# Optimization experiments

Measured on AMD Instinct MI355X. Metric: run time of the kernel, lower is better.

## Reference

```python
import jax, jax.numpy as jnp
import numpy as np

TAU = 0.8
LAMBDA_BALANCE = 0.05
EPS = 1e-8


def setup_inputs() -> dict:
    key = jax.random.key(0)
    ks = jax.random.split(key, 8)
    B, Din, Dh, Dout, E = 8192, 1024, 2048, 1024, 8
    x = jax.random.normal(ks[0], (B, Din), jnp.float32)
    # gumbel noise for F.gumbel_softmax: g = -log(-log(U)), U~Uniform(0,1)
    u = jax.random.uniform(ks[1], (B, E), jnp.float32, 1e-6, 1.0 - 1e-6)
    gumbel = -jnp.log(-jnp.log(u))
    gate_w = jax.random.normal(ks[2], (Din, E), jnp.float32) * 0.02
    gate_b = jnp.zeros((E,), jnp.float32)
    w1 = jax.random.normal(ks[3], (E, Din, Dh), jnp.float32) * (1.0 / np.sqrt(Din))
    b1 = jnp.zeros((E, Dh), jnp.float32)
    w2 = jax.random.normal(ks[4], (E, Dh, Dout), jnp.float32) * (1.0 / np.sqrt(Dh))
    b2 = jnp.zeros((E, Dout), jnp.float32)
    return dict(x=x, gumbel=gumbel, gate_w=gate_w, gate_b=gate_b,
                w1=w1, b1=b1, w2=w2, b2=b2)


def reference(x, gumbel, gate_w, gate_b, w1, b1, w2, b2):
    # gating logits [B, E]
    logits = x @ gate_w + gate_b
    # gumbel-softmax (soft), tau=0.8 -> selection probs (selection_policy='soft')
    probs = jax.nn.softmax((logits + gumbel) / TAU, axis=1)
    # load-balancing auxiliary loss
    router_probs = jax.nn.softmax(logits / TAU, axis=1)
    importance = router_probs.mean(axis=0)  # [E]
    load = probs.mean(axis=0)               # [E]
    importance_cv = jnp.std(importance, ddof=1) / (importance.mean() + EPS)
    load_cv = jnp.std(load, ddof=1) / (load.mean() + EPS)
    E = probs.shape[1]
    switch_loss = E * jnp.sum(importance * load)
    aux_loss = (switch_loss + importance_cv + load_cv) * LAMBDA_BALANCE
    # dense all-expert MLP stack: h [E,B,Dh], eo [E,B,Dout]
    h = jax.nn.relu(jnp.einsum('bd,edh->ebh', x, w1) + b1[:, None, :])
    eo = jnp.einsum('ebh,eho->ebo', h, w2) + b2[:, None, :]
    # bmm combine: expert_outputs [B, Dout, E] @ probs [B, E, 1] -> [B, Dout]
    output = jnp.einsum('ebo,be->bo', eo, probs)
    return output, aux_loss
```

## Files before the change

kernel.cpp:

```cpp
#include <hip/hip_runtime.h>

typedef __attribute__((ext_vector_type(4))) float f4;
typedef __attribute__((ext_vector_type(8))) short s8;

__device__ inline float b2f(unsigned int u) {
    unsigned int v = u << 16;
    float f;
    __builtin_memcpy(&f, &v, 4);
    return f;
}
__device__ inline unsigned short f2b(float f) {
    unsigned int u;
    __builtin_memcpy(&u, &f, 4);
    unsigned int r = u + 0x7fffu + ((u >> 16) & 1u);
    return (unsigned short)(r >> 16);
}
__device__ inline void async16(const void* g, void* l) {
    __builtin_amdgcn_global_load_lds(
        (const __attribute__((address_space(1))) unsigned int*)g,
        (__attribute__((address_space(3))) unsigned int*)l, 16, 0, 0);
}

#define B_ROWS 8192
#define DIN 1024
#define DH 2048
#define DOUT 1024
#define NE 8
#define NCAT 16384

__global__ __launch_bounds__(64) void detect_dtype(const unsigned short* __restrict__ p, int* __restrict__ flag)
{
    const int lane = threadIdx.x;
    int sane = 0;
    for (int i = lane; i < 4096; i += 64) {
        const float a = fabsf(b2f(p[i]));
        if (a > 1e-30f && a < 1e3f) sane++;
    }
    for (int off = 32; off; off >>= 1) sane += __shfl_xor(sane, off, 64);
    if (lane == 0) *flag = (sane < 3600) ? 1 : 0;
}

__global__ __launch_bounds__(256) void normalize_kernel(const void* __restrict__ src,
                                                        unsigned short* __restrict__ dst,
                                                        const int* __restrict__ flag, int n)
{
    const int i = blockIdx.x * 256 + threadIdx.x;
    if (i >= n) return;
    if (*flag) dst[i] = f2b(((const float*)src)[i]);
    else       dst[i] = ((const unsigned short*)src)[i];
}

__global__ __launch_bounds__(256) void gating_kernel(
    const unsigned short* __restrict__ x, const unsigned short* __restrict__ gum,
    const unsigned short* __restrict__ gw, const unsigned short* __restrict__ gb,
    float* __restrict__ probs, float* __restrict__ partials)
{
    const int t = threadIdx.x, wave = t >> 6, lane = t & 63;
    float sp = 0.f, sr = 0.f;
    const int base = blockIdx.x * 32 + wave * 8;
    for (int rr = 0; rr < 8; rr++) {
        const int b = base + rr;
        float acc[8];
#pragma unroll
        for (int e = 0; e < 8; e++) acc[e] = 0.f;
        for (int kk = 0; kk < 16; kk++) {
            const int k = kk * 64 + lane;
            const float xv = b2f(x[(size_t)b * DIN + k]);
            const uint4 wv = *(const uint4*)(gw + (size_t)k * 8);
            acc[0] += xv * b2f(wv.x & 0xffffu); acc[1] += xv * b2f(wv.x >> 16);
            acc[2] += xv * b2f(wv.y & 0xffffu); acc[3] += xv * b2f(wv.y >> 16);
            acc[4] += xv * b2f(wv.z & 0xffffu); acc[5] += xv * b2f(wv.z >> 16);
            acc[6] += xv * b2f(wv.w & 0xffffu); acc[7] += xv * b2f(wv.w >> 16);
        }
#pragma unroll
        for (int e = 0; e < 8; e++)
            for (int off = 32; off; off >>= 1) acc[e] += __shfl_xor(acc[e], off, 64);
        float lg[8], p1[8], p2[8];
        float m1 = -1e30f, m2 = -1e30f;
#pragma unroll
        for (int e = 0; e < 8; e++) {
            lg[e] = acc[e] + b2f(gb[e]);
            p1[e] = (lg[e] + b2f(gum[(size_t)b * 8 + e])) * 1.25f;
            p2[e] = lg[e] * 1.25f;
            m1 = fmaxf(m1, p1[e]); m2 = fmaxf(m2, p2[e]);
        }
        float s1 = 0.f, s2 = 0.f;
#pragma unroll
        for (int e = 0; e < 8; e++) {
            p1[e] = expf(p1[e] - m1); s1 += p1[e];
            p2[e] = expf(p2[e] - m2); s2 += p2[e];
        }
        const float i1 = 1.f / s1, i2 = 1.f / s2;
        if (lane < 8) {
            const float pv = p1[lane] * i1;
            probs[(size_t)b * 8 + lane] = pv;
            sp += pv;
            sr += p2[lane] * i2;
        }
    }
    __shared__ float red[4][16];
    if (lane < 8) { red[wave][lane] = sp; red[wave][8 + lane] = sr; }
    __syncthreads();
    if (t < 16)
        partials[blockIdx.x * 16 + t] = red[0][t] + red[1][t] + red[2][t] + red[3][t];
}

__global__ void aux_finalize(const float* __restrict__ partials, void* __restrict__ outp,
                             const int* __restrict__ flag)
{
    __shared__ float fin[16];
    const int t = threadIdx.x;
    if (t < 16) {
        float s = 0.f;
        for (int i = 0; i < 256; i++) s += partials[i * 16 + t];
        fin[t] = s;
    }
    __syncthreads();
    if (t == 0) {
        float ld[8], im[8];
        for (int e = 0; e < 8; e++) { ld[e] = fin[e] / 8192.f; im[e] = fin[8 + e] / 8192.f; }
        float mi = 0.f, ml = 0.f;
        for (int e = 0; e < 8; e++) { mi += im[e]; ml += ld[e]; }
        mi *= 0.125f; ml *= 0.125f;
        float vi = 0.f, vl = 0.f, sw = 0.f;
        for (int e = 0; e < 8; e++) {
            vi += (im[e] - mi) * (im[e] - mi);
            vl += (ld[e] - ml) * (ld[e] - ml);
            sw += im[e] * ld[e];
        }
        const float cvi = sqrtf(vi / 7.f) / (mi + 1e-8f);
        const float cvl = sqrtf(vl / 7.f) / (ml + 1e-8f);
        const float aux = (8.f * sw + cvi + cvl) * 0.05f;
        if (*flag) ((float*)outp)[8388608] = aux;
        else       ((unsigned short*)outp)[8388608] = f2b(aux);
    }
}

__global__ __launch_bounds__(256) void transpose_cvt(
    const void* __restrict__ src, unsigned short* __restrict__ out,
    int R, int C, int ldOut, size_t outEStride, const int* __restrict__ flag)
{
    __shared__ unsigned short tile[64][65];
    const int e = blockIdx.z;
    const size_t eoff = (size_t)e * R * C;
    unsigned short* op = out + (size_t)e * outEStride;
    const int fl = *flag;
    const int tx = threadIdx.x, ty = threadIdx.y;
    const int r0 = blockIdx.y * 64, c0 = blockIdx.x * 64;
    if (fl) {
        const float* in = (const float*)src + eoff;
#pragma unroll
        for (int i = 0; i < 16; i++) {
            const int r = ty + i * 4;
            tile[r][tx] = f2b(in[(size_t)(r0 + r) * C + c0 + tx]);
        }
    } else {
        const unsigned short* in = (const unsigned short*)src + eoff;
#pragma unroll
        for (int i = 0; i < 16; i++) {
            const int r = ty + i * 4;
            tile[r][tx] = in[(size_t)(r0 + r) * C + c0 + tx];
        }
    }
    __syncthreads();
#pragma unroll
    for (int i = 0; i < 16; i++) {
        const int c = ty + i * 4;
        op[(size_t)(c0 + c) * ldOut + r0 + tx] = tile[tx][c];
    }
}

__global__ __launch_bounds__(256) void gemm_h(
    const unsigned short* __restrict__ A,
    const unsigned short* __restrict__ Bt,
    const unsigned short* __restrict__ bias,
    const float* __restrict__ probs,
    unsigned short* __restrict__ outH)
{
    constexpr int K = DIN;
    __shared__ __align__(16) char smem[32768];

    const int t = threadIdx.x;
    const int m0 = blockIdx.x * 128, n0 = blockIdx.y * 128;
    const int wave = t >> 6, lane = t & 63;
    const int wm = wave >> 1, wn = wave & 1;
    const int quad = lane >> 4, l16 = lane & 15;

    f4 acc[4][4];
#pragma unroll
    for (int i = 0; i < 4; i++)
#pragma unroll
        for (int j = 0; j < 4; j++) { acc[i][j][0] = 0.f; acc[i][j][1] = 0.f; acc[i][j][2] = 0.f; acc[i][j][3] = 0.f; }

    const int rA = t >> 2;
    const int cb = (t & 3) * 16;
    const char* pA0 = (const char*)(A + (size_t)(m0 + rA) * K) + cb;
    const char* pA1 = pA0 + (size_t)64 * K * 2;
    const char* pB0 = (const char*)(Bt + (size_t)(n0 + rA) * K) + cb;
    const char* pB1 = pB0 + (size_t)64 * K * 2;

    int aoff[4], boff[4];
#pragma unroll
    for (int i = 0; i < 4; i++) {
        aoff[i] = ((wm * 64 + i * 16 + l16) * 32 + quad * 8) * 2;
        boff[i] = ((wn * 64 + i * 16 + l16) * 32 + quad * 8) * 2;
    }

    auto stage = [&](int buf, int k0) {
        const size_t kb = (size_t)k0 * 2;
        char* s = smem + buf * 16384;
        async16(pA0 + kb, s + t * 16);
        async16(pA1 + kb, s + 4096 + t * 16);
        async16(pB0 + kb, s + 8192 + t * 16);
        async16(pB1 + kb, s + 12288 + t * 16);
    };

    stage(0, 0);
    __syncthreads();
    int cur = 0;
    for (int k0 = 0; k0 < K; k0 += 32) {
        if (k0 + 32 < K) stage(cur ^ 1, k0 + 32);
        const char* s = smem + cur * 16384;
        s8 av[4], bv[4];
#pragma unroll
        for (int i = 0; i < 4; i++) av[i] = *(const s8*)(s + aoff[i]);
#pragma unroll
        for (int j = 0; j < 4; j++) bv[j] = *(const s8*)(s + 8192 + boff[j]);
#pragma unroll
        for (int i = 0; i < 4; i++)
#pragma unroll
            for (int j = 0; j < 4; j++)
                acc[i][j] = __builtin_amdgcn_mfma_f32_16x16x32_bf16(av[i], bv[j], acc[i][j], 0, 0, 0);
        __syncthreads();
        cur ^= 1;
    }

#pragma unroll
    for (int i = 0; i < 4; i++) {
        const int gmB = m0 + wm * 64 + i * 16 + quad * 4;
#pragma unroll
        for (int j = 0; j < 4; j++) {
            const int gn = n0 + wn * 64 + j * 16 + l16;
            const int e = gn >> 11;
            const float bval = b2f(bias[gn]);
#pragma unroll
            for (int r = 0; r < 4; r++) {
                const int gm = gmB + r;
                const float pb = probs[(size_t)gm * 8 + e];
                float v = acc[i][j][r] + bval;
                v = fmaxf(v, 0.f) * pb;
                outH[(size_t)gm * NCAT + gn] = f2b(v);
            }
        }
    }
}

__global__ __launch_bounds__(256) void gemm_out_sk(
    const unsigned short* __restrict__ A,
    const unsigned short* __restrict__ Bt,
    float* __restrict__ partial, int rows)
{
    constexpr int K = NCAT;
    __shared__ __align__(16) char smem[32768];

    const int t = threadIdx.x;
    const int m0 = blockIdx.x * 128, n0 = blockIdx.y * 128;
    const int nks = gridDim.z;
    const int klen = K / nks;
    const int kstart = blockIdx.z * klen;
    const int kend = kstart + klen;
    const int wave = t >> 6, lane = t & 63;
    const int wm = wave >> 1, wn = wave & 1;
    const int quad = lane >> 4, l16 = lane & 15;

    f4 acc[4][4];
#pragma unroll
    for (int i = 0; i < 4; i++)
#pragma unroll
        for (int j = 0; j < 4; j++) { acc[i][j][0] = 0.f; acc[i][j][1] = 0.f; acc[i][j][2] = 0.f; acc[i][j][3] = 0.f; }

    const int rA = t >> 2;
    const int cb = (t & 3) * 16;
    const char* pA0 = (const char*)(A + (size_t)(m0 + rA) * K) + cb;
    const char* pA1 = pA0 + (size_t)64 * K * 2;
    const char* pB0 = (const char*)(Bt + (size_t)(n0 + rA) * K) + cb;
    const char* pB1 = pB0 + (size_t)64 * K * 2;

    int aoff[4], boff[4];
#pragma unroll
    for (int i = 0; i < 4; i++) {
        aoff[i] = ((wm * 64 + i * 16 + l16) * 32 + quad * 8) * 2;
        boff[i] = ((wn * 64 + i * 16 + l16) * 32 + quad * 8) * 2;
    }

    auto stage = [&](int buf, int k0) {
        const size_t kb = (size_t)k0 * 2;
        char* s = smem + buf * 16384;
        async16(pA0 + kb, s + t * 16);
        async16(pA1 + kb, s + 4096 + t * 16);
        async16(pB0 + kb, s + 8192 + t * 16);
        async16(pB1 + kb, s + 12288 + t * 16);
    };

    stage(0, kstart);
    __syncthreads();
    int cur = 0;
    for (int k0 = kstart; k0 < kend; k0 += 32) {
        if (k0 + 32 < kend) stage(cur ^ 1, k0 + 32);
        const char* s = smem + cur * 16384;
        s8 av[4], bv[4];
#pragma unroll
        for (int i = 0; i < 4; i++) av[i] = *(const s8*)(s + aoff[i]);
#pragma unroll
        for (int j = 0; j < 4; j++) bv[j] = *(const s8*)(s + 8192 + boff[j]);
#pragma unroll
        for (int i = 0; i < 4; i++)
#pragma unroll
            for (int j = 0; j < 4; j++)
                acc[i][j] = __builtin_amdgcn_mfma_f32_16x16x32_bf16(av[i], bv[j], acc[i][j], 0, 0, 0);
        __syncthreads();
        cur ^= 1;
    }

    float* pp = partial + (size_t)blockIdx.z * rows * DOUT;
#pragma unroll
    for (int i = 0; i < 4; i++) {
        const int gmB = m0 + wm * 64 + i * 16 + quad * 4;
#pragma unroll
        for (int j = 0; j < 4; j++) {
            const int gn = n0 + wn * 64 + j * 16 + l16;
#pragma unroll
            for (int r = 0; r < 4; r++)
                pp[(size_t)(gmB + r) * DOUT + gn] = acc[i][j][r];
        }
    }
}

__global__ __launch_bounds__(256) void out_finalize(
    const float* __restrict__ partial, const unsigned short* __restrict__ b2,
    const float* __restrict__ probs, void* __restrict__ outp, size_t outOff,
    const int* __restrict__ flag, int rows, int nks)
{
    const int idx = blockIdx.x * 256 + threadIdx.x;
    if (idx >= rows * DOUT) return;
    const int m = idx >> 10, n = idx & (DOUT - 1);
    float v = 0.f;
    for (int ks = 0; ks < nks; ks++)
        v += partial[(size_t)ks * rows * DOUT + idx];
    const f4 p0 = *(const f4*)(probs + (size_t)m * 8);
    const f4 p1 = *(const f4*)(probs + (size_t)m * 8 + 4);
    v += p0[0] * b2f(b2[n])            + p0[1] * b2f(b2[DOUT + n])
       + p0[2] * b2f(b2[2 * DOUT + n]) + p0[3] * b2f(b2[3 * DOUT + n])
       + p1[0] * b2f(b2[4 * DOUT + n]) + p1[1] * b2f(b2[5 * DOUT + n])
       + p1[2] * b2f(b2[6 * DOUT + n]) + p1[3] * b2f(b2[7 * DOUT + n]);
    const size_t oi = outOff + ((size_t)m * DOUT) + n;
    if (*flag) ((float*)outp)[oi] = v;
    else       ((unsigned short*)outp)[oi] = f2b(v);
}

extern "C" void kernel_launch(void* const* d_in, const int* in_sizes, int n_in,
                              void* d_out, int out_size, void* d_ws, size_t ws_size,
                              hipStream_t stream)
{
    const void* x   = d_in[0];
    const void* gum = d_in[1];
    const void* gw  = d_in[2];
    const void* gb  = d_in[3];
    const void* w1  = d_in[4];
    const void* b1  = d_in[5];
    const void* w2  = d_in[6];
    const void* b2  = d_in[7];

    char* ws = (char*)d_ws;
    size_t cur = 0;
    auto alloc = [&](size_t bytes) { size_t p = cur; cur = (cur + bytes + 255) & ~(size_t)255; return p; };

    int* flag              = (int*)(ws + alloc(256));
    float* probs           = (float*)(ws + alloc(8192 * 8 * 4));
    float* partials        = (float*)(ws + alloc(256 * 16 * 4));
    unsigned short* xn     = (unsigned short*)(ws + alloc((size_t)B_ROWS * DIN * 2));
    unsigned short* gumn   = (unsigned short*)(ws + alloc((size_t)B_ROWS * 8 * 2));
    unsigned short* gwn    = (unsigned short*)(ws + alloc((size_t)DIN * 8 * 2));
    unsigned short* gbn    = (unsigned short*)(ws + alloc(8 * 2));
    unsigned short* b1n    = (unsigned short*)(ws + alloc((size_t)NE * DH * 2));
    unsigned short* b2n    = (unsigned short*)(ws + alloc((size_t)NE * DOUT * 2));
    unsigned short* w1Tcat = (unsigned short*)(ws + alloc((size_t)NCAT * DIN * 2));
    unsigned short* w2Tcat = (unsigned short*)(ws + alloc((size_t)DOUT * NCAT * 2));
    const size_t fixed = cur;

    int R = B_ROWS, KS = 2;
    for (;;) {
        KS = 8192 / R; if (KS < 2) KS = 2;
        const size_t need = fixed + (size_t)R * (NCAT * 2) + (size_t)KS * R * DOUT * 4;
        if (R <= 256 || need <= ws_size) break;
        R >>= 1;
    }
    unsigned short* Hcat = (unsigned short*)(ws + fixed);
    float* partial = (float*)(ws + fixed + (size_t)R * (NCAT * 2));

    detect_dtype<<<1, 64, 0, stream>>>((const unsigned short*)x, flag);

    normalize_kernel<<<(B_ROWS * DIN + 255) / 256, 256, 0, stream>>>(x, xn, flag, B_ROWS * DIN);
    normalize_kernel<<<(B_ROWS * 8 + 255) / 256, 256, 0, stream>>>(gum, gumn, flag, B_ROWS * 8);
    normalize_kernel<<<(DIN * 8 + 255) / 256, 256, 0, stream>>>(gw, gwn, flag, DIN * 8);
    normalize_kernel<<<1, 256, 0, stream>>>(gb, gbn, flag, 8);
    normalize_kernel<<<(NE * DH + 255) / 256, 256, 0, stream>>>(b1, b1n, flag, NE * DH);
    normalize_kernel<<<(NE * DOUT + 255) / 256, 256, 0, stream>>>(b2, b2n, flag, NE * DOUT);

    gating_kernel<<<256, 256, 0, stream>>>(xn, gumn, gwn, gbn, probs, partials);
    aux_finalize<<<1, 64, 0, stream>>>(partials, d_out, flag);

    transpose_cvt<<<dim3(DH / 64, DIN / 64, NE), dim3(64, 4), 0, stream>>>(
        w1, w1Tcat, DIN, DH, DIN, (size_t)DH * DIN, flag);
    transpose_cvt<<<dim3(DOUT / 64, DH / 64, NE), dim3(64, 4), 0, stream>>>(
        w2, w2Tcat, DH, DOUT, NCAT, (size_t)DH, flag);

    for (int c0 = 0; c0 < B_ROWS; c0 += R) {
        gemm_h<<<dim3(R / 128, NCAT / 128), 256, 0, stream>>>(
            xn + (size_t)c0 * DIN, w1Tcat, b1n, probs + (size_t)c0 * 8, Hcat);
        gemm_out_sk<<<dim3(R / 128, DOUT / 128, KS), 256, 0, stream>>>(
            Hcat, w2Tcat, partial, R);
        out_finalize<<<(R * DOUT) / 256, 256, 0, stream>>>(
            partial, b2n, probs + (size_t)c0 * 8, d_out, (size_t)c0 * DOUT, flag, R, KS);
    }
}
```

Baseline: 1.018 ms.

## Replace 128x128 GEMMs with a shared 256x256 swizzled-LDS MFMA kernel

Merges the two bf16 MFMA GEMMs into one templated kernel. It uses 256x256 output tiles, 512 threads, K-tiles of 64 and a 128 KB double-buffered LDS with XOR swizzling. The kernel also adds explicit vmcnt waits, wave priority raising around the MFMA bursts, and block-index swizzling for the first GEMM. The aim is more operand reuse per byte loaded, fewer LDS bank conflicts, and better overlap of loads with math. The cost is higher register and LDS pressure per block, so occupancy is limited, and the split-K and row-chunk sizing is retuned to match.

```diff
diff --git a/kernel.cpp b/kernel.cpp
--- a/kernel.cpp
+++ b/kernel.cpp
@@ -170,168 +170,148 @@
     }
 }
 
-__global__ __launch_bounds__(256) void gemm_h(
+#define MFMA16(a, b, c) __builtin_amdgcn_mfma_f32_16x16x32_bf16(a, b, c, 0, 0, 0)
+
+template<int K, int EPI>
+__global__ __launch_bounds__(512, 2) void gemm256(
     const unsigned short* __restrict__ A,
     const unsigned short* __restrict__ Bt,
     const unsigned short* __restrict__ bias,
     const float* __restrict__ probs,
-    unsigned short* __restrict__ outH)
-{
-    constexpr int K = DIN;
-    __shared__ __align__(16) char smem[32768];
-
+    unsigned short* __restrict__ outH,
+    float* __restrict__ partial,
+    int rows, int klen, int SWZ)
+{
+    __shared__ __align__(16) char smem[131072];
     const int t = threadIdx.x;
-    const int m0 = blockIdx.x * 128, n0 = blockIdx.y * 128;
-    const int wave = t >> 6, lane = t & 63;
-    const int wm = wave >> 1, wn = wave & 1;
-    const int quad = lane >> 4, l16 = lane & 15;
-
-    f4 acc[4][4];
-#pragma unroll
-    for (int i = 0; i < 4; i++)
+    const int w = t >> 6, l = t & 63;
+    const int l15 = l & 15, q = l >> 4;
+    const int wm = w >> 2, wn = w & 3;
+
+    int bx = blockIdx.x, by = blockIdx.y;
+    if (SWZ) {
+        const int n = gridDim.x * gridDim.y;
+        int bid = by * gridDim.x + bx;
+        const int c = n >> 3;
+        bid = (bid & 7) * c + (bid >> 3);
+        bx = bid % gridDim.x; by = bid / gridDim.x;
+    }
+    const int m0 = bx * 256, n0 = by * 256;
+    const int kstart = blockIdx.z * klen;
+    const int NT = klen >> 6;
+
+    const int srow = l >> 3;
+    const int swz = (l & 7) ^ srow;
+    const char* pa[4]; const char* pb[4];
+#pragma unroll
+    for (int i = 0; i < 4; i++) {
+        const int ra = m0 + (w * 4 + i) * 8 + srow;
+        const int rb = n0 + (w * 4 + i) * 8 + srow;
+        pa[i] = (const char*)(A  + (size_t)ra * K + kstart + swz * 8);
+        pb[i] = (const char*)(Bt + (size_t)rb * K + kstart + swz * 8);
+    }
+
+    auto stage = [&](int kt, int bsel) {
+        char* Ab = smem + bsel * 65536;
+        char* Bb = Ab + 32768;
+        const size_t kb = (size_t)kt * 128;
+#pragma unroll
+        for (int i = 0; i < 4; i++) async16(pa[i] + kb, Ab + (w * 4 + i) * 1024);
+#pragma unroll
+        for (int i = 0; i < 4; i++) async16(pb[i] + kb, Bb + (w * 4 + i) * 1024);
+    };
+
+    f4 acc[8][4];
+#pragma unroll
+    for (int i = 0; i < 8; i++)
 #pragma unroll
         for (int j = 0; j < 4; j++) { acc[i][j][0] = 0.f; acc[i][j][1] = 0.f; acc[i][j][2] = 0.f; acc[i][j][3] = 0.f; }
 
-    const int rA = t >> 2;
-    const int cb = (t & 3) * 16;
-    const char* pA0 = (const char*)(A + (size_t)(m0 + rA) * K) + cb;
-    const char* pA1 = pA0 + (size_t)64 * K * 2;
-    const char* pB0 = (const char*)(Bt + (size_t)(n0 + rA) * K) + cb;
-    const char* pB1 = pB0 + (size_t)64 * K * 2;
-
-    int aoff[4], boff[4];
-#pragma unroll
-    for (int i = 0; i < 4; i++) {
-        aoff[i] = ((wm * 64 + i * 16 + l16) * 32 + quad * 8) * 2;
-        boff[i] = ((wn * 64 + i * 16 + l16) * 32 + quad * 8) * 2;
-    }
-
-    auto stage = [&](int buf, int k0) {
-        const size_t kb = (size_t)k0 * 2;
-        char* s = smem + buf * 16384;
-        async16(pA0 + kb, s + t * 16);
-        async16(pA1 + kb, s + 4096 + t * 16);
-        async16(pB0 + kb, s + 8192 + t * 16);
-        async16(pB1 + kb, s + 12288 + t * 16);
-    };
+    const int arow0 = (wm * 128 + l15) * 128;
+    const int brow0 = (wn * 64 + l15) * 128;
+    int sz[2];
+#pragma unroll
+    for (int kh = 0; kh < 2; kh++) sz[kh] = (((kh * 4 + q) ^ (l & 7)) << 4);
 
     stage(0, 0);
-    __syncthreads();
-    int cur = 0;
-    for (int k0 = 0; k0 < K; k0 += 32) {
-        if (k0 + 32 < K) stage(cur ^ 1, k0 + 32);
-        const char* s = smem + cur * 16384;
-        s8 av[4], bv[4];
-#pragma unroll
-        for (int i = 0; i < 4; i++) av[i] = *(const s8*)(s + aoff[i]);
-#pragma unroll
-        for (int j = 0; j < 4; j++) bv[j] = *(const s8*)(s + 8192 + boff[j]);
-#pragma unroll
-        for (int i = 0; i < 4; i++)
-#pragma unroll
-            for (int j = 0; j < 4; j++)
-                acc[i][j] = __builtin_amdgcn_mfma_f32_16x16x32_bf16(av[i], bv[j], acc[i][j], 0, 0, 0);
-        __syncthreads();
-        cur ^= 1;
-    }
-
-#pragma unroll
-    for (int i = 0; i < 4; i++) {
-        const int gmB = m0 + wm * 64 + i * 16 + quad * 4;
-#pragma unroll
-        for (int j = 0; j < 4; j++) {
-            const int gn = n0 + wn * 64 + j * 16 + l16;
+    stage(1, 1);
+
+    for (int kt = 0; kt < NT; ++kt) {
+        if (kt + 1 < NT) asm volatile("s_waitcnt vmcnt(8)" ::: "memory");
+        else             asm volatile("s_waitcnt vmcnt(0)" ::: "memory");
+        __builtin_amdgcn_s_barrier();
+        const char* Ab = smem + (kt & 1) * 65536;
+        const char* Bb = Ab + 32768;
+        s8 Af[4][2], Bf[4][2];
+#pragma unroll
+        for (int mf = 0; mf < 4; mf++)
+#pragma unroll
+            for (int kh = 0; kh < 2; kh++)
+                Af[mf][kh] = *(const s8*)(Ab + arow0 + mf * 2048 + sz[kh]);
+#pragma unroll
+        for (int nf = 0; nf < 4; nf++)
+#pragma unroll
+            for (int kh = 0; kh < 2; kh++)
+                Bf[nf][kh] = *(const s8*)(Bb + brow0 + nf * 2048 + sz[kh]);
+        __builtin_amdgcn_s_setprio(1);
+#pragma unroll
+        for (int mf = 0; mf < 4; mf++)
+#pragma unroll
+            for (int nf = 0; nf < 4; nf++) {
+                acc[mf][nf] = MFMA16(Af[mf][0], Bf[nf][0], acc[mf][nf]);
+                acc[mf][nf] = MFMA16(Af[mf][1], Bf[nf][1], acc[mf][nf]);
+            }
+        __builtin_amdgcn_s_setprio(0);
+#pragma unroll
+        for (int mf = 0; mf < 4; mf++)
+#pragma unroll
+            for (int kh = 0; kh < 2; kh++)
+                Af[mf][kh] = *(const s8*)(Ab + arow0 + (mf + 4) * 2048 + sz[kh]);
+        __builtin_amdgcn_s_setprio(1);
+#pragma unroll
+        for (int mf = 0; mf < 4; mf++)
+#pragma unroll
+            for (int nf = 0; nf < 4; nf++) {
+                acc[mf + 4][nf] = MFMA16(Af[mf][0], Bf[nf][0], acc[mf + 4][nf]);
+                acc[mf + 4][nf] = MFMA16(Af[mf][1], Bf[nf][1], acc[mf + 4][nf]);
+            }
+        __builtin_amdgcn_s_setprio(0);
+        asm volatile("s_waitcnt lgkmcnt(0)" ::: "memory");
+        __builtin_amdgcn_sched_barrier(0);
+        __builtin_amdgcn_s_barrier();
+        if (kt + 2 < NT) stage(kt + 2, kt & 1);
+    }
+
+    if (EPI == 0) {
+#pragma unroll
+        for (int nf = 0; nf < 4; nf++) {
+            const int gn = n0 + wn * 64 + nf * 16 + l15;
             const int e = gn >> 11;
             const float bval = b2f(bias[gn]);
 #pragma unroll
-            for (int r = 0; r < 4; r++) {
-                const int gm = gmB + r;
-                const float pb = probs[(size_t)gm * 8 + e];
-                float v = acc[i][j][r] + bval;
-                v = fmaxf(v, 0.f) * pb;
-                outH[(size_t)gm * NCAT + gn] = f2b(v);
+            for (int mf = 0; mf < 8; mf++) {
+                const int gmB = m0 + wm * 128 + mf * 16 + q * 4;
+#pragma unroll
+                for (int r = 0; r < 4; r++) {
+                    const int gm = gmB + r;
+                    const float pv = probs[(size_t)gm * 8 + e];
+                    const float v = fmaxf(acc[mf][nf][r] + bval, 0.f) * pv;
+                    outH[(size_t)gm * NCAT + gn] = f2b(v);
+                }
             }
         }
-    }
-}
-
-__global__ __launch_bounds__(256) void gemm_out_sk(
-    const unsigned short* __restrict__ A,
-    const unsigned short* __restrict__ Bt,
-    float* __restrict__ partial, int rows)
-{
-    constexpr int K = NCAT;
-    __shared__ __align__(16) char smem[32768];
-
-    const int t = threadIdx.x;
-    const int m0 = blockIdx.x * 128, n0 = blockIdx.y * 128;
-    const int nks = gridDim.z;
-    const int klen = K / nks;
-    const int kstart = blockIdx.z * klen;
-    const int kend = kstart + klen;
-    const int wave = t >> 6, lane = t & 63;
-    const int wm = wave >> 1, wn = wave & 1;
-    const int quad = lane >> 4, l16 = lane & 15;
-
-    f4 acc[4][4];
-#pragma unroll
-    for (int i = 0; i < 4; i++)
-#pragma unroll
-        for (int j = 0; j < 4; j++) { acc[i][j][0] = 0.f; acc[i][j][1] = 0.f; acc[i][j][2] = 0.f; acc[i][j][3] = 0.f; }
-
-    const int rA = t >> 2;
-    const int cb = (t & 3) * 16;
-    const char* pA0 = (const char*)(A + (size_t)(m0 + rA) * K) + cb;
-    const char* pA1 = pA0 + (size_t)64 * K * 2;
-    const char* pB0 = (const char*)(Bt + (size_t)(n0 + rA) * K) + cb;
-    const char* pB1 = pB0 + (size_t)64 * K * 2;
-
-    int aoff[4], boff[4];
-#pragma unroll
-    for (int i = 0; i < 4; i++) {
-        aoff[i] = ((wm * 64 + i * 16 + l16) * 32 + quad * 8) * 2;
-        boff[i] = ((wn * 64 + i * 16 + l16) * 32 + quad * 8) * 2;
-    }
-
-    auto stage = [&](int buf, int k0) {
-        const size_t kb = (size_t)k0 * 2;
-        char* s = smem + buf * 16384;
-        async16(pA0 + kb, s + t * 16);
-        async16(pA1 + kb, s + 4096 + t * 16);
-        async16(pB0 + kb, s + 8192 + t * 16);
-        async16(pB1 + kb, s + 12288 + t * 16);
-    };
-
-    stage(0, kstart);
-    __syncthreads();
-    int cur = 0;
-    for (int k0 = kstart; k0 < kend; k0 += 32) {
-        if (k0 + 32 < kend) stage(cur ^ 1, k0 + 32);
-        const char* s = smem + cur * 16384;
-        s8 av[4], bv[4];
-#pragma unroll
-        for (int i = 0; i < 4; i++) av[i] = *(const s8*)(s + aoff[i]);
-#pragma unroll
-        for (int j = 0; j < 4; j++) bv[j] = *(const s8*)(s + 8192 + boff[j]);
-#pragma unroll
-        for (int i = 0; i < 4; i++)
-#pragma unroll
-            for (int j = 0; j < 4; j++)
-                acc[i][j] = __builtin_amdgcn_mfma_f32_16x16x32_bf16(av[i], bv[j], acc[i][j], 0, 0, 0);
-        __syncthreads();
-        cur ^= 1;
-    }
-
-    float* pp = partial + (size_t)blockIdx.z * rows * DOUT;
-#pragma unroll
-    for (int i = 0; i < 4; i++) {
-        const int gmB = m0 + wm * 64 + i * 16 + quad * 4;
-#pragma unroll
-        for (int j = 0; j < 4; j++) {
-            const int gn = n0 + wn * 64 + j * 16 + l16;
-#pragma unroll
-            for (int r = 0; r < 4; r++)
-                pp[(size_t)(gmB + r) * DOUT + gn] = acc[i][j][r];
+    } else {
+        float* pp = partial + (size_t)blockIdx.z * rows * DOUT;
+#pragma unroll
+        for (int mf = 0; mf < 8; mf++) {
+            const int gmB = m0 + wm * 128 + mf * 16 + q * 4;
+#pragma unroll
+            for (int nf = 0; nf < 4; nf++) {
+                const int gn = n0 + wn * 64 + nf * 16 + l15;
+#pragma unroll
+                for (int r = 0; r < 4; r++)
+                    pp[(size_t)(gmB + r) * DOUT + gn] = acc[mf][nf][r];
+            }
         }
     }
 }
@@ -388,13 +368,14 @@
     unsigned short* w2Tcat = (unsigned short*)(ws + alloc((size_t)DOUT * NCAT * 2));
     const size_t fixed = cur;
 
-    int R = B_ROWS, KS = 2;
+    int R = B_ROWS, KS;
     for (;;) {
-        KS = 8192 / R; if (KS < 2) KS = 2;
+        KS = 16384 / R;
         const size_t need = fixed + (size_t)R * (NCAT * 2) + (size_t)KS * R * DOUT * 4;
-        if (R <= 256 || need <= ws_size) break;
+        if (R <= 512 || need <= ws_size) break;
         R >>= 1;
     }
+    const int klen = 16384 / KS;
     unsigned short* Hcat = (unsigned short*)(ws + fixed);
     float* partial = (float*)(ws + fixed + (size_t)R * (NCAT * 2));
 
@@ -416,10 +397,12 @@
         w2, w2Tcat, DH, DOUT, NCAT, (size_t)DH, flag);
 
     for (int c0 = 0; c0 < B_ROWS; c0 += R) {
-        gemm_h<<<dim3(R / 128, NCAT / 128), 256, 0, stream>>>(
-            xn + (size_t)c0 * DIN, w1Tcat, b1n, probs + (size_t)c0 * 8, Hcat);
-        gemm_out_sk<<<dim3(R / 128, DOUT / 128, KS), 256, 0, stream>>>(
-            Hcat, w2Tcat, partial, R);
+        gemm256<DIN, 0><<<dim3(R / 256, NCAT / 256, 1), 512, 0, stream>>>(
+            xn + (size_t)c0 * DIN, w1Tcat, b1n, probs + (size_t)c0 * 8, Hcat,
+            nullptr, R, DIN, 1);
+        gemm256<NCAT, 1><<<dim3(R / 256, DOUT / 256, KS), 512, 0, stream>>>(
+            Hcat, w2Tcat, nullptr, nullptr, nullptr,
+            partial, R, klen, 0);
         out_finalize<<<(R * DOUT) / 256, 256, 0, stream>>>(
             partial, b2n, probs + (size_t)c0 * 8, d_out, (size_t)c0 * DOUT, flag, R, KS);
     }
```

New measurement: 1.057 ms. 3.8% more time.
